# Kernel optimization log

Measured on AMD Instinct MI355X. Metric: run time of the kernel, lower is better.

Reference implementation:

```python
import jax, jax.numpy as jnp
import numpy as np

B, F, D = 16384, 64, 32
H = 256            # deep_intermediate_size
HO = 128           # higher_order_features_size
NPAIR = F * (F - 1) // 2
CIN = HO + NPAIR + D
OUT = 1


def setup_inputs() -> dict:
    key = jax.random.key(0)
    ks = jax.random.split(key, 12)
    s = 0.02
    return {
        'x':   jax.random.normal(ks[0], (B, F, D), jnp.float32),
        'W1':  jax.random.normal(ks[1], (F * D, H), jnp.float32) * s,
        'b1':  jnp.zeros((H,), jnp.float32),
        'W2':  jax.random.normal(ks[2], (H, H), jnp.float32) * s,
        'b2':  jnp.zeros((H,), jnp.float32),
        'W3':  jax.random.normal(ks[3], (H, HO), jnp.float32) * s,
        'b3':  jnp.zeros((HO,), jnp.float32),
        'Wc1': jax.random.normal(ks[4], (CIN, 256), jnp.float32) * s,
        'bc1': jnp.zeros((256,), jnp.float32),
        'Wc2': jax.random.normal(ks[5], (256, OUT), jnp.float32) * s,
        'bc2': jnp.zeros((OUT,), jnp.float32),
    }


def reference(x, W1, b1, W2, b2, W3, b3, Wc1, bc1, Wc2, bc2):
    b, f, d = x.shape
    # second-order interactions: Gram matrix + upper-triangular extraction
    # (replaces the O(F^2) python loop of bmm's in the original)
    gram = jnp.einsum('bid,bjd->bij', x, x)          # (B, F, F)
    iu, ju = jnp.triu_indices(f, k=1)                # row-major i<j order, matches the loop
    soi = gram[:, iu, ju]                            # (B, F*(F-1)/2)
    # original writes so_int into a fresh non-grad tensor -> detached
    soi = jax.lax.stop_gradient(soi)

    # deep processor (3-layer MLP with SELU; dropout inactive at eval)
    h = jax.nn.selu(x.reshape(b, f * d) @ W1 + b1)
    h = jax.nn.selu(h @ W2 + b2)
    hoi = h @ W3 + b3                                # (B, HO)

    first_order = x.sum(axis=1)                      # (B, D)

    cin = jnp.concatenate([hoi, soi, first_order], axis=1)  # (B, CIN)
    c = jax.nn.relu(cin @ Wc1 + bc1)
    return c @ Wc2 + bc2                             # (B, OUT)
```

## Files before the change

### kernel.cpp

```cpp
#include <hip/hip_runtime.h>
#include <hip/hip_bf16.h>

#define BATCH 16384
#define F_DIM 64
#define D_DIM 32
#define H_DIM 256
#define HO_DIM 128
#define NPAIR 2016
#define CIN_DIM 2176

typedef __hip_bfloat16 bf16;
using bf16x8 = __attribute__((ext_vector_type(8))) __bf16;
using f32x4  = __attribute__((ext_vector_type(4))) float;

__device__ inline float selu_f(float v) {
    const float scale = 1.0507009873554805f;
    const float alpha = 1.6732632423543772f;
    return v > 0.f ? scale * v : scale * alpha * (__expf(v) - 1.f);
}

__device__ inline void gload16(const void* g, void* l) {
    __builtin_amdgcn_global_load_lds(
        (const __attribute__((address_space(1))) void*)g,
        (__attribute__((address_space(3))) void*)l,
        16, 0, 0);
}

__global__ void prep(const float* __restrict__ W1, const float* __restrict__ W2,
                     const float* __restrict__ W3, const float* __restrict__ Wc1,
                     bf16* __restrict__ W1T, bf16* __restrict__ W2T,
                     bf16* __restrict__ W3Tsw, bf16* __restrict__ Wc1T) {
    int bid = blockIdx.x, tid = threadIdx.x;
    if (bid < 2048) {
        int i = bid * 256 + tid;
        int n = i & 255, k = i >> 8;
        W1T[(size_t)n * 2048 + k] = __float2bfloat16(W1[i]);
    } else if (bid < 2304) {
        int i = (bid - 2048) * 256 + tid;
        int n = i & 255, k = i >> 8;
        W2T[n * 256 + k] = __float2bfloat16(W2[i]);
    } else if (bid < 2432) {
        int i = (bid - 2304) * 256 + tid;
        int k = i >> 7, n = i & 127;
        W3Tsw[n * 256 + (((k >> 3) ^ (n & 7)) * 8) + (k & 7)] = __float2bfloat16(W3[i]);
    } else {
        int i = (bid - 2432) * 256 + tid;
        int n = i & 255, k = i >> 8;
        Wc1T[(size_t)n * 2176 + k] = __float2bfloat16(Wc1[i]);
    }
}

__global__ __launch_bounds__(512, 2) void gram_mlp1(
    const float* __restrict__ x, const bf16* __restrict__ W1T,
    const float* __restrict__ b1, bf16* __restrict__ cin, bf16* __restrict__ h1) {
    constexpr int K = 2048;
    __shared__ __align__(16) char smraw[81920];
    bf16* Abuf0 = (bf16*)smraw;
    bf16* Abuf1 = (bf16*)(smraw + 8192);
    bf16* Bbuf0 = (bf16*)(smraw + 16384);
    bf16* Bbuf1 = (bf16*)(smraw + 49152);

    const int tid = threadIdx.x;
    const int w = tid >> 6, l = tid & 63;
    const int lr = l & 15, lk = l >> 4;
    const int wm = w >> 2, wn = w & 3;
    const int blk = blockIdx.x;
    const int batch0 = blk * 64 + w * 8;

    bf16x8 xa[8][4];
    bf16* mysoi = (bf16*)(smraw + w * 4096);
    const int pi[10] = {0,0,0,0,1,1,1,2,2,3};
    const int pj[10] = {0,1,2,3,1,2,3,2,3,3};

    float4 pf[2][8];
#pragma unroll
    for (int ti = 0; ti < 4; ++ti) {
        const float* p = x + (size_t)batch0 * 2048 + (ti * 16 + lr) * 32 + lk * 8;
        pf[0][ti * 2]     = *(const float4*)p;
        pf[0][ti * 2 + 1] = *(const float4*)(p + 4);
    }

#pragma unroll
    for (int bb = 0; bb < 8; ++bb) {
        if (bb < 7) {
#pragma unroll
            for (int ti = 0; ti < 4; ++ti) {
                const float* p = x + (size_t)(batch0 + bb + 1) * 2048 + (ti * 16 + lr) * 32 + lk * 8;
                pf[(bb + 1) & 1][ti * 2]     = *(const float4*)p;
                pf[(bb + 1) & 1][ti * 2 + 1] = *(const float4*)(p + 4);
            }
        }
        float fsum[8];
#pragma unroll
        for (int j = 0; j < 8; ++j) fsum[j] = 0.f;
#pragma unroll
        for (int ti = 0; ti < 4; ++ti) {
            float4 f0 = pf[bb & 1][ti * 2];
            float4 f1 = pf[bb & 1][ti * 2 + 1];
            bf16x8 t;
            t[0] = (__bf16)f0.x; t[1] = (__bf16)f0.y; t[2] = (__bf16)f0.z; t[3] = (__bf16)f0.w;
            t[4] = (__bf16)f1.x; t[5] = (__bf16)f1.y; t[6] = (__bf16)f1.z; t[7] = (__bf16)f1.w;
            xa[bb][ti] = t;
            fsum[0] += f0.x; fsum[1] += f0.y; fsum[2] += f0.z; fsum[3] += f0.w;
            fsum[4] += f1.x; fsum[5] += f1.y; fsum[6] += f1.z; fsum[7] += f1.w;
        }
#pragma unroll
        for (int m = 1; m < 16; m <<= 1)
#pragma unroll
            for (int j = 0; j < 8; ++j)
                fsum[j] += __shfl_xor(fsum[j], m, 64);
        if (lr == 0) {
            bf16x8 fv;
#pragma unroll
            for (int j = 0; j < 8; ++j) fv[j] = (__bf16)fsum[j];
            *(bf16x8*)(cin + (size_t)(batch0 + bb) * CIN_DIM + (HO_DIM + NPAIR) + lk * 8) = fv;
        }
        f32x4 zero = {0.f, 0.f, 0.f, 0.f};
#pragma unroll
        for (int p = 0; p < 10; ++p) {
            f32x4 g = __builtin_amdgcn_mfma_f32_16x16x32_bf16(xa[bb][pi[p]], xa[bb][pj[p]], zero, 0, 0, 0);
            int ib = pi[p] * 16 + lk * 4;
            int j  = pj[p] * 16 + lr;
#pragma unroll
            for (int r = 0; r < 4; ++r) {
                int i = ib + r;
                if (j > i) {
                    int idx = (i * (127 - i)) / 2 + (j - i - 1);
                    mysoi[idx] = __float2bfloat16(g[r]);
                }
            }
        }
        const uint4* s4 = (const uint4*)mysoi;
        uint4* dst = (uint4*)(cin + (size_t)(batch0 + bb) * CIN_DIM + HO_DIM);
        for (int c = l; c < 252; c += 64) dst[c] = s4[c];
    }

    __syncthreads();

    const bf16* gBs[4];
#pragma unroll
    for (int s = 0; s < 4; ++s) {
        int col = s * 64 + (tid >> 3);
        gBs[s] = W1T + (size_t)col * K + (((tid & 7) ^ (col & 7)) * 8);
    }
    int aoff[2][2], boff[4][2];
#pragma unroll
    for (int fm = 0; fm < 2; ++fm) {
        int arow = wm * 32 + fm * 16 + lr;
#pragma unroll
        for (int kk = 0; kk < 2; ++kk)
            aoff[fm][kk] = arow * 64 + (((kk * 4 + lk) ^ (arow & 7)) * 8);
    }
#pragma unroll
    for (int fn = 0; fn < 4; ++fn) {
        int bcol = wn * 64 + fn * 16 + lr;
#pragma unroll
        for (int kk = 0; kk < 2; ++kk)
            boff[fn][kk] = bcol * 64 + (((kk * 4 + lk) ^ (bcol & 7)) * 8);
    }

    f32x4 acc[2][4];
#pragma unroll
    for (int fm = 0; fm < 2; ++fm)
#pragma unroll
        for (int fn = 0; fn < 4; ++fn)
            acc[fm][fn] = (f32x4){0.f, 0.f, 0.f, 0.f};

#define WRITEA(tt, DST) { \
    const int f0_ = 2 * (tt); \
    const int lrA_ = f0_ & 15, lrB_ = (f0_ + 1) & 15; \
    int delta_ = (lr == lrA_) ? 0 : ((lr == lrB_) ? 1 : -1); \
    if (delta_ >= 0) { \
        int cs_ = delta_ * 4 + lk; \
        _Pragma("unroll") \
        for (int bb_ = 0; bb_ < 8; ++bb_) { \
            int row_ = w * 8 + bb_; \
            *(bf16x8*)((DST) + row_ * 64 + ((cs_ ^ (row_ & 7)) * 8)) = xa[bb_][(tt) >> 3]; \
        } } }

    WRITEA(0, Abuf0);
#pragma unroll
    for (int s = 0; s < 4; ++s)
        gload16(gBs[s], Bbuf0 + (s * 512 + tid) * 8);
    __syncthreads();

#pragma unroll
    for (int t = 0; t < 32; ++t) {
        bf16* Ac = (t & 1) ? Abuf1 : Abuf0;
        bf16* Bc = (t & 1) ? Bbuf1 : Bbuf0;
        bf16* An = (t & 1) ? Abuf0 : Abuf1;
        bf16* Bn = (t & 1) ? Bbuf0 : Bbuf1;
        if (t < 31) {
#pragma unroll
            for (int s = 0; s < 4; ++s)
                gload16(gBs[s] + (size_t)(t + 1) * 64, Bn + (s * 512 + tid) * 8);
        }
        bf16x8 a[2][2], bfr[4][2];
#pragma unroll
        for (int fm = 0; fm < 2; ++fm)
#pragma unroll
            for (int kk = 0; kk < 2; ++kk)
                a[fm][kk] = *(const bf16x8*)(Ac + aoff[fm][kk]);
#pragma unroll
        for (int fn = 0; fn < 4; ++fn)
#pragma unroll
            for (int kk = 0; kk < 2; ++kk)
                bfr[fn][kk] = *(const bf16x8*)(Bc + boff[fn][kk]);
#pragma unroll
        for (int kk = 0; kk < 2; ++kk)
#pragma unroll
            for (int fm = 0; fm < 2; ++fm)
#pragma unroll
                for (int fn = 0; fn < 4; ++fn)
                    acc[fm][fn] = __builtin_amdgcn_mfma_f32_16x16x32_bf16(
                        a[fm][kk], bfr[fn][kk], acc[fm][fn], 0, 0, 0);
        if (t < 31) WRITEA(t + 1, An);
        __syncthreads();
    }
#undef WRITEA

#pragma unroll
    for (int fm = 0; fm < 2; ++fm) {
#pragma unroll
        for (int fn = 0; fn < 4; ++fn) {
            int col = wn * 64 + fn * 16 + lr;
            float bv = b1[col];
#pragma unroll
            for (int r = 0; r < 4; ++r) {
                float v = selu_f(acc[fm][fn][r] + bv);
                int row = blk * 64 + wm * 32 + fm * 16 + lk * 4 + r;
                h1[(size_t)row * 256 + col] = __float2bfloat16(v);
            }
        }
    }
}

__global__ __launch_bounds__(512, 2) void mlp23(
    const bf16* __restrict__ h1, const bf16* __restrict__ W2T, const float* __restrict__ b2,
    const bf16* __restrict__ W3Tsw, const float* __restrict__ b3, bf16* __restrict__ cin) {
    __shared__ __align__(16) char smraw[147456];
    bf16* Abuf0 = (bf16*)smraw;
    bf16* Abuf1 = (bf16*)(smraw + 8192);
    bf16* Bbuf0 = (bf16*)(smraw + 16384);
    bf16* Bbuf1 = (bf16*)(smraw + 49152);
    bf16* w3l   = (bf16*)(smraw + 81920);
    bf16* h2sw  = (bf16*)smraw;

    const int tid = threadIdx.x;
    const int w = tid >> 6, l = tid & 63;
    const int lr = l & 15, lk = l >> 4;
    const int wm = w >> 2, wn = w & 3;
    const int rowblk = blockIdx.x * 64;
    const int srow = tid >> 3, sks = tid & 7;

#pragma unroll
    for (int s = 0; s < 8; ++s)
        gload16(W3Tsw + (size_t)(s * 512 + tid) * 8, w3l + (s * 512 + tid) * 8);

    const bf16* gA = h1 + (size_t)(rowblk + srow) * 256 + ((sks ^ (srow & 7)) * 8);
    const bf16* gBs[4];
#pragma unroll
    for (int s = 0; s < 4; ++s) {
        int col = s * 64 + srow;
        gBs[s] = W2T + (size_t)col * 256 + ((sks ^ (col & 7)) * 8);
    }
    int aoff[2][2], boff[4][2];
#pragma unroll
    for (int fm = 0; fm < 2; ++fm) {
        int arow = wm * 32 + fm * 16 + lr;
#pragma unroll
        for (int kk = 0; kk < 2; ++kk)
            aoff[fm][kk] = arow * 64 + (((kk * 4 + lk) ^ (arow & 7)) * 8);
    }
#pragma unroll
    for (int fn = 0; fn < 4; ++fn) {
        int bcol = wn * 64 + fn * 16 + lr;
#pragma unroll
        for (int kk = 0; kk < 2; ++kk)
            boff[fn][kk] = bcol * 64 + (((kk * 4 + lk) ^ (bcol & 7)) * 8);
    }

    f32x4 acc[2][4];
#pragma unroll
    for (int fm = 0; fm < 2; ++fm)
#pragma unroll
        for (int fn = 0; fn < 4; ++fn)
            acc[fm][fn] = (f32x4){0.f, 0.f, 0.f, 0.f};

    gload16(gA, Abuf0 + tid * 8);
#pragma unroll
    for (int s = 0; s < 4; ++s)
        gload16(gBs[s], Bbuf0 + (s * 512 + tid) * 8);
    __syncthreads();

#pragma unroll
    for (int t = 0; t < 4; ++t) {
        bf16* Ac = (t & 1) ? Abuf1 : Abuf0;
        bf16* Bc = (t & 1) ? Bbuf1 : Bbuf0;
        bf16* An = (t & 1) ? Abuf0 : Abuf1;
        bf16* Bn = (t & 1) ? Bbuf0 : Bbuf1;
        if (t < 3) {
            gload16(gA + (size_t)(t + 1) * 64, An + tid * 8);
#pragma unroll
            for (int s = 0; s < 4; ++s)
                gload16(gBs[s] + (size_t)(t + 1) * 64, Bn + (s * 512 + tid) * 8);
        }
        bf16x8 a[2][2], bfr[4][2];
#pragma unroll
        for (int fm = 0; fm < 2; ++fm)
#pragma unroll
            for (int kk = 0; kk < 2; ++kk)
                a[fm][kk] = *(const bf16x8*)(Ac + aoff[fm][kk]);
#pragma unroll
        for (int fn = 0; fn < 4; ++fn)
#pragma unroll
            for (int kk = 0; kk < 2; ++kk)
                bfr[fn][kk] = *(const bf16x8*)(Bc + boff[fn][kk]);
#pragma unroll
        for (int kk = 0; kk < 2; ++kk)
#pragma unroll
            for (int fm = 0; fm < 2; ++fm)
#pragma unroll
                for (int fn = 0; fn < 4; ++fn)
                    acc[fm][fn] = __builtin_amdgcn_mfma_f32_16x16x32_bf16(
                        a[fm][kk], bfr[fn][kk], acc[fm][fn], 0, 0, 0);
        __syncthreads();
    }

#pragma unroll
    for (int fm = 0; fm < 2; ++fm) {
#pragma unroll
        for (int fn = 0; fn < 4; ++fn) {
            int col = wn * 64 + fn * 16 + lr;
            float bv = b2[col];
#pragma unroll
            for (int r = 0; r < 4; ++r) {
                float v = selu_f(acc[fm][fn][r] + bv);
                int row = wm * 32 + fm * 16 + lk * 4 + r;
                h2sw[row * 256 + (((col >> 3) ^ (row & 7)) * 8) + (col & 7)] = __float2bfloat16(v);
            }
        }
    }
    __syncthreads();

    f32x4 acc2[2][2];
#pragma unroll
    for (int fm = 0; fm < 2; ++fm)
#pragma unroll
        for (int fn = 0; fn < 2; ++fn)
            acc2[fm][fn] = (f32x4){0.f, 0.f, 0.f, 0.f};
#pragma unroll
    for (int ks = 0; ks < 8; ++ks) {
        bf16x8 a2[2], b2f[2];
#pragma unroll
        for (int fm = 0; fm < 2; ++fm) {
            int arow = wm * 32 + fm * 16 + lr;
            a2[fm] = *(const bf16x8*)(h2sw + arow * 256 + (((ks * 4 + lk) ^ (arow & 7)) * 8));
        }
#pragma unroll
        for (int fn = 0; fn < 2; ++fn) {
            int ncol = wn * 32 + fn * 16 + lr;
            b2f[fn] = *(const bf16x8*)(w3l + ncol * 256 + (((ks * 4 + lk) ^ (ncol & 7)) * 8));
        }
#pragma unroll
        for (int fm = 0; fm < 2; ++fm)
#pragma unroll
            for (int fn = 0; fn < 2; ++fn)
                acc2[fm][fn] = __builtin_amdgcn_mfma_f32_16x16x32_bf16(
                    a2[fm], b2f[fn], acc2[fm][fn], 0, 0, 0);
    }
#pragma unroll
    for (int fm = 0; fm < 2; ++fm) {
#pragma unroll
        for (int fn = 0; fn < 2; ++fn) {
            int col = wn * 32 + fn * 16 + lr;
            float bv = b3[col];
#pragma unroll
            for (int r = 0; r < 4; ++r) {
                float v = acc2[fm][fn][r] + bv;
                int row = rowblk + wm * 32 + fm * 16 + lk * 4 + r;
                cin[(size_t)row * CIN_DIM + col] = __float2bfloat16(v);
            }
        }
    }
}

template<int K, int N>
__global__ __launch_bounds__(512) void gemm_head(
    const bf16* __restrict__ A,
    const bf16* __restrict__ BT,
    const float* __restrict__ bias,
    const float* __restrict__ Wc2, const float* __restrict__ bc2,
    float* __restrict__ Out)
{
    constexpr int BK = 64;
    constexpr int NT = K / BK;
    constexpr int FN = N / 64;
    constexpr int BST = (N * 8) / 512;

    __shared__ __align__(16) bf16 Abuf[2][64 * BK];
    __shared__ __align__(16) bf16 Bbuf[2][N * BK];
    __shared__ float red[4][64];

    const int tid = threadIdx.x;
    const int w = tid >> 6, l = tid & 63;
    const int wm = w >> 2, wn = w & 3;
    const int lr = l & 15, lk = l >> 4;
    const int rowblk = blockIdx.x * 64;
    const int srow = tid >> 3, sks = tid & 7;

    const bf16* gAb = A + (size_t)(rowblk + srow) * K + ((sks ^ (srow & 7)) * 8);
    const bf16* gBs[BST];
#pragma unroll
    for (int s = 0; s < BST; ++s) {
        int col = s * 64 + srow;
        gBs[s] = BT + (size_t)col * K + ((sks ^ (col & 7)) * 8);
    }

    int aoff[2][2], boff[FN][2];
#pragma unroll
    for (int fm = 0; fm < 2; ++fm) {
        int arow = wm * 32 + fm * 16 + lr;
#pragma unroll
        for (int kk = 0; kk < 2; ++kk)
            aoff[fm][kk] = arow * BK + (((kk * 4 + lk) ^ (arow & 7)) * 8);
    }
#pragma unroll
    for (int fn = 0; fn < FN; ++fn) {
        int bcol = wn * (FN * 16) + fn * 16 + lr;
#pragma unroll
        for (int kk = 0; kk < 2; ++kk)
            boff[fn][kk] = bcol * BK + (((kk * 4 + lk) ^ (bcol & 7)) * 8);
    }

    f32x4 acc[2][FN];
#pragma unroll
    for (int fm = 0; fm < 2; ++fm)
#pragma unroll
        for (int fn = 0; fn < FN; ++fn)
            acc[fm][fn] = (f32x4){0.f, 0.f, 0.f, 0.f};

    auto stage = [&](int buf, int t) {
        gload16(gAb + (size_t)t * BK, &Abuf[buf][tid * 8]);
#pragma unroll
        for (int s = 0; s < BST; ++s)
            gload16(gBs[s] + (size_t)t * BK, &Bbuf[buf][(s * 512 + tid) * 8]);
    };

    stage(0, 0);
    __syncthreads();

    int cur = 0;
    for (int t = 0; t < NT; ++t) {
        if (t + 1 < NT) stage(cur ^ 1, t + 1);
        bf16x8 a[2][2], bfr[FN][2];
#pragma unroll
        for (int fm = 0; fm < 2; ++fm)
#pragma unroll
            for (int kk = 0; kk < 2; ++kk)
                a[fm][kk] = *(const bf16x8*)&Abuf[cur][aoff[fm][kk]];
#pragma unroll
        for (int fn = 0; fn < FN; ++fn)
#pragma unroll
            for (int kk = 0; kk < 2; ++kk)
                bfr[fn][kk] = *(const bf16x8*)&Bbuf[cur][boff[fn][kk]];
#pragma unroll
        for (int kk = 0; kk < 2; ++kk)
#pragma unroll
            for (int fm = 0; fm < 2; ++fm)
#pragma unroll
                for (int fn = 0; fn < FN; ++fn)
                    acc[fm][fn] = __builtin_amdgcn_mfma_f32_16x16x32_bf16(
                        a[fm][kk], bfr[fn][kk], acc[fm][fn], 0, 0, 0);
        __syncthreads();
        cur ^= 1;
    }

    float part[2][4];
#pragma unroll
    for (int fm = 0; fm < 2; ++fm)
#pragma unroll
        for (int r = 0; r < 4; ++r) part[fm][r] = 0.f;
#pragma unroll
    for (int fm = 0; fm < 2; ++fm) {
#pragma unroll
        for (int fn = 0; fn < FN; ++fn) {
            int col = wn * (FN * 16) + fn * 16 + lr;
            float bv = bias[col];
            float wv = Wc2[col];
#pragma unroll
            for (int r = 0; r < 4; ++r) {
                float v = acc[fm][fn][r] + bv;
                v = fmaxf(v, 0.f);
                part[fm][r] += v * wv;
            }
        }
    }
#pragma unroll
    for (int fm = 0; fm < 2; ++fm)
#pragma unroll
        for (int r = 0; r < 4; ++r)
#pragma unroll
            for (int m = 1; m < 16; m <<= 1)
                part[fm][r] += __shfl_xor(part[fm][r], m, 64);
    if (lr == 0) {
#pragma unroll
        for (int fm = 0; fm < 2; ++fm)
#pragma unroll
            for (int r = 0; r < 4; ++r)
                red[wn][wm * 32 + fm * 16 + lk * 4 + r] = part[fm][r];
    }
    __syncthreads();
    if (tid < 64)
        Out[rowblk + tid] = red[0][tid] + red[1][tid] + red[2][tid] + red[3][tid] + bc2[0];
}

extern "C" void kernel_launch(void* const* d_in, const int* in_sizes, int n_in,
                              void* d_out, int out_size, void* d_ws, size_t ws_size,
                              hipStream_t stream) {
    const float* x   = (const float*)d_in[0];
    const float* W1  = (const float*)d_in[1];
    const float* b1  = (const float*)d_in[2];
    const float* W2  = (const float*)d_in[3];
    const float* b2  = (const float*)d_in[4];
    const float* W3  = (const float*)d_in[5];
    const float* b3  = (const float*)d_in[6];
    const float* Wc1 = (const float*)d_in[7];
    const float* bc1 = (const float*)d_in[8];
    const float* Wc2 = (const float*)d_in[9];
    const float* bc2 = (const float*)d_in[10];
    float* out = (float*)d_out;

    char* ws = (char*)d_ws;
    bf16* W1T   = (bf16*)ws; ws += (size_t)256 * 2048 * 2;
    bf16* W2T   = (bf16*)ws; ws += (size_t)256 * 256 * 2;
    bf16* W3Tsw = (bf16*)ws; ws += (size_t)128 * 256 * 2;
    bf16* Wc1T  = (bf16*)ws; ws += (size_t)256 * 2176 * 2;
    bf16* h1    = (bf16*)ws; ws += (size_t)BATCH * H_DIM * 2;
    bf16* cin   = (bf16*)ws; ws += (size_t)BATCH * CIN_DIM * 2;

    prep<<<4608, 256, 0, stream>>>(W1, W2, W3, Wc1, W1T, W2T, W3Tsw, Wc1T);
    gram_mlp1<<<256, 512, 0, stream>>>(x, W1T, b1, cin, h1);
    mlp23<<<256, 512, 0, stream>>>(h1, W2T, b2, W3Tsw, b3, cin);
    gemm_head<2176, 256><<<256, 512, 0, stream>>>(cin, Wc1T, bc1, Wc2, bc2, out);
}
```

Baseline: 123.3 us.

## Fuse Gram tiles directly into head GEMM, drop materialized cin buffer

The head's first layer is split by input segment. The second-order part is computed in the gram kernel by streaming Gram tiles from LDS straight into MFMA against a padded, tile-ordered copy of Wc1, and the first-order part is added in the same pass. The partial result is stored as fp32 z. The higher-order part and the ReLU/Wc2 reduction are fused into the MLP23 kernel, which removes the large bf16 cin round trip and one launch. In exchange the padded K grows to 2560 with about 20% wasted MACs, the gram kernel uses more LDS and drops to one block per CU, and an fp32 z buffer adds traffic.

```diff
diff --git a/kernel.cpp b/kernel.cpp
--- a/kernel.cpp
+++ b/kernel.cpp
@@ -7,7 +7,7 @@
 #define H_DIM 256
 #define HO_DIM 128
 #define NPAIR 2016
-#define CIN_DIM 2176
+#define KSOI 2560
 
 typedef __hip_bfloat16 bf16;
 using bf16x8 = __attribute__((ext_vector_type(8))) __bf16;
@@ -26,10 +26,17 @@
         16, 0, 0);
 }
 
+__device__ inline int soi_swz(int dw, int row) {
+    return dw ^ (((dw >> 5) & 3) << 3) ^ ((row & 7) << 2);
+}
+
 __global__ void prep(const float* __restrict__ W1, const float* __restrict__ W2,
                      const float* __restrict__ W3, const float* __restrict__ Wc1,
                      bf16* __restrict__ W1T, bf16* __restrict__ W2T,
-                     bf16* __restrict__ W3Tsw, bf16* __restrict__ Wc1T) {
+                     bf16* __restrict__ W3Tsw, bf16* __restrict__ Wc1p,
+                     bf16* __restrict__ Wc1hT, bf16* __restrict__ Wc1fT) {
+    const int TI[10] = {0,0,0,0,1,1,1,2,2,3};
+    const int TJ[10] = {0,1,2,3,1,2,3,2,3,3};
     int bid = blockIdx.x, tid = threadIdx.x;
     if (bid < 2048) {
         int i = bid * 256 + tid;
@@ -43,22 +50,40 @@
         int i = (bid - 2304) * 256 + tid;
         int k = i >> 7, n = i & 127;
         W3Tsw[n * 256 + (((k >> 3) ^ (n & 7)) * 8) + (k & 7)] = __float2bfloat16(W3[i]);
+    } else if (bid < 2688) {
+        int n = bid - 2432;
+        for (int kp = tid; kp < KSOI; kp += 256) {
+            int t = kp >> 8, s = kp & 255;
+            int gi = TI[t] * 16 + (s >> 4);
+            int gj = TJ[t] * 16 + (s & 15);
+            float v = 0.f;
+            if (gi < gj) {
+                int pidx = (gi * (127 - gi)) / 2 + (gj - gi - 1);
+                v = Wc1[(size_t)(HO_DIM + pidx) * 256 + n];
+            }
+            Wc1p[(size_t)n * KSOI + kp] = __float2bfloat16(v);
+        }
+    } else if (bid < 2816) {
+        int i = (bid - 2688) * 256 + tid;
+        int n = i >> 7, k = i & 127;
+        Wc1hT[n * 128 + k] = __float2bfloat16(Wc1[(size_t)k * 256 + n]);
     } else {
-        int i = (bid - 2432) * 256 + tid;
-        int n = i & 255, k = i >> 8;
-        Wc1T[(size_t)n * 2176 + k] = __float2bfloat16(Wc1[i]);
+        int i = (bid - 2816) * 256 + tid;
+        int n = i >> 5, k = i & 31;
+        Wc1fT[n * 32 + k] = __float2bfloat16(Wc1[(size_t)(HO_DIM + NPAIR + k) * 256 + n]);
     }
 }
 
-__global__ __launch_bounds__(512, 2) void gram_mlp1(
-    const float* __restrict__ x, const bf16* __restrict__ W1T,
-    const float* __restrict__ b1, bf16* __restrict__ cin, bf16* __restrict__ h1) {
-    constexpr int K = 2048;
-    __shared__ __align__(16) char smraw[81920];
-    bf16* Abuf0 = (bf16*)smraw;
-    bf16* Abuf1 = (bf16*)(smraw + 8192);
-    bf16* Bbuf0 = (bf16*)(smraw + 16384);
-    bf16* Bbuf1 = (bf16*)(smraw + 49152);
+__global__ __launch_bounds__(512, 1) void gram_z_mlp1(
+    const float* __restrict__ x, const bf16* __restrict__ Wc1p,
+    const bf16* __restrict__ Wc1fT, const bf16* __restrict__ W1T,
+    const float* __restrict__ b1, float* __restrict__ z, bf16* __restrict__ h1) {
+    constexpr int TI[10] = {0,0,0,0,1,1,1,2,2,3};
+    constexpr int TJ[10] = {0,1,2,3,1,2,3,2,3,3};
+    __shared__ __align__(16) char smraw[135168];
+    bf16* Afirst = (bf16*)(smraw + 131072);
+    bf16* Bsoi0  = (bf16*)(smraw + 65536);
+    bf16* Bsoi1  = (bf16*)(smraw + 98304);
 
     const int tid = threadIdx.x;
     const int w = tid >> 6, l = tid & 63;
@@ -66,12 +91,9 @@
     const int wm = w >> 2, wn = w & 3;
     const int blk = blockIdx.x;
     const int batch0 = blk * 64 + w * 8;
+    const int srow = tid >> 3, sks = tid & 7;
 
     bf16x8 xa[8][4];
-    bf16* mysoi = (bf16*)(smraw + w * 4096);
-    const int pi[10] = {0,0,0,0,1,1,1,2,2,3};
-    const int pj[10] = {0,1,2,3,1,2,3,2,3,3};
-
     float4 pf[2][8];
 #pragma unroll
     for (int ti = 0; ti < 4; ++ti) {
@@ -79,7 +101,6 @@
         pf[0][ti * 2]     = *(const float4*)p;
         pf[0][ti * 2 + 1] = *(const float4*)(p + 4);
     }
-
 #pragma unroll
     for (int bb = 0; bb < 8; ++bb) {
         if (bb < 7) {
@@ -113,35 +134,134 @@
             bf16x8 fv;
 #pragma unroll
             for (int j = 0; j < 8; ++j) fv[j] = (__bf16)fsum[j];
-            *(bf16x8*)(cin + (size_t)(batch0 + bb) * CIN_DIM + (HO_DIM + NPAIR) + lk * 8) = fv;
-        }
+            *(bf16x8*)(Afirst + (w * 8 + bb) * 32 + lk * 8) = fv;
+        }
+    }
+
+    const bf16* gBs[4];
+#pragma unroll
+    for (int s = 0; s < 4; ++s) {
+        int col = s * 64 + srow;
+        gBs[s] = Wc1p + (size_t)col * KSOI + ((sks ^ (col & 7)) * 8);
+    }
+    {
         f32x4 zero = {0.f, 0.f, 0.f, 0.f};
 #pragma unroll
-        for (int p = 0; p < 10; ++p) {
-            f32x4 g = __builtin_amdgcn_mfma_f32_16x16x32_bf16(xa[bb][pi[p]], xa[bb][pj[p]], zero, 0, 0, 0);
-            int ib = pi[p] * 16 + lk * 4;
-            int j  = pj[p] * 16 + lr;
+        for (int bb = 0; bb < 8; ++bb) {
+            f32x4 g = __builtin_amdgcn_mfma_f32_16x16x32_bf16(xa[bb][0], xa[bb][0], zero, 0, 0, 0);
+            int rowb = w * 8 + bb;
 #pragma unroll
             for (int r = 0; r < 4; ++r) {
-                int i = ib + r;
-                if (j > i) {
-                    int idx = (i * (127 - i)) / 2 + (j - i - 1);
-                    mysoi[idx] = __float2bfloat16(g[r]);
+                int i = lk * 4 + r;
+                int dw = i * 8 + (lr >> 1);
+                *(bf16*)(smraw + rowb * 512 + soi_swz(dw, rowb) * 4 + (lr & 1) * 2) =
+                    __float2bfloat16(g[r]);
+            }
+        }
+#pragma unroll
+        for (int s = 0; s < 4; ++s)
+            gload16(gBs[s], Bsoi0 + (s * 512 + tid) * 8);
+    }
+    __syncthreads();
+
+    f32x4 acc[2][4];
+    {
+        bf16x8 af[2], bf_[4];
+#pragma unroll
+        for (int fm = 0; fm < 2; ++fm) {
+            int row = wm * 32 + fm * 16 + lr;
+            af[fm] = *(const bf16x8*)(Afirst + row * 32 + lk * 8);
+        }
+#pragma unroll
+        for (int fn = 0; fn < 4; ++fn) {
+            int col = wn * 64 + fn * 16 + lr;
+            bf_[fn] = *(const bf16x8*)(Wc1fT + col * 32 + lk * 8);
+        }
+        f32x4 zero = {0.f, 0.f, 0.f, 0.f};
+#pragma unroll
+        for (int fm = 0; fm < 2; ++fm)
+#pragma unroll
+            for (int fn = 0; fn < 4; ++fn)
+                acc[fm][fn] = __builtin_amdgcn_mfma_f32_16x16x32_bf16(af[fm], bf_[fn], zero, 0, 0, 0);
+    }
+
+#pragma unroll
+    for (int c = 0; c < 40; ++c) {
+        const int t = c >> 2;
+        char* at = smraw + ((t & 1) ? 32768 : 0);
+        bf16* Bc = (c & 1) ? Bsoi1 : Bsoi0;
+        bf16* Bn = (c & 1) ? Bsoi0 : Bsoi1;
+        if (c < 39) {
+#pragma unroll
+            for (int s = 0; s < 4; ++s)
+                gload16(gBs[s] + (c + 1) * 64, Bn + (s * 512 + tid) * 8);
+        }
+        bf16x8 a[2][2], bfr[4][2];
+#pragma unroll
+        for (int kk2 = 0; kk2 < 2; ++kk2) {
+            const int ks = (c & 3) * 2 + kk2;
+#pragma unroll
+            for (int fm = 0; fm < 2; ++fm) {
+                int row = wm * 32 + fm * 16 + lr;
+                int i = ks * 2 + (lk >> 1);
+                int dw = i * 8 + (lk & 1) * 4;
+                a[fm][kk2] = *(const bf16x8*)(at + row * 512 + soi_swz(dw, row) * 4);
+            }
+#pragma unroll
+            for (int fn = 0; fn < 4; ++fn) {
+                int bcol = wn * 64 + fn * 16 + lr;
+                bfr[fn][kk2] = *(const bf16x8*)(Bc + bcol * 64 + (((kk2 * 4 + lk) ^ (bcol & 7)) * 8));
+            }
+        }
+#pragma unroll
+        for (int kk2 = 0; kk2 < 2; ++kk2)
+#pragma unroll
+            for (int fm = 0; fm < 2; ++fm)
+#pragma unroll
+                for (int fn = 0; fn < 4; ++fn)
+                    acc[fm][fn] = __builtin_amdgcn_mfma_f32_16x16x32_bf16(
+                        a[fm][kk2], bfr[fn][kk2], acc[fm][fn], 0, 0, 0);
+        if ((c & 3) == 3 && t < 9) {
+            char* an = smraw + (((t + 1) & 1) ? 32768 : 0);
+            f32x4 zero = {0.f, 0.f, 0.f, 0.f};
+#pragma unroll
+            for (int bb = 0; bb < 8; ++bb) {
+                f32x4 g = __builtin_amdgcn_mfma_f32_16x16x32_bf16(
+                    xa[bb][TI[t + 1]], xa[bb][TJ[t + 1]], zero, 0, 0, 0);
+                int rowb = w * 8 + bb;
+#pragma unroll
+                for (int r = 0; r < 4; ++r) {
+                    int i = lk * 4 + r;
+                    int dw = i * 8 + (lr >> 1);
+                    *(bf16*)(an + rowb * 512 + soi_swz(dw, rowb) * 4 + (lr & 1) * 2) =
+                        __float2bfloat16(g[r]);
                 }
             }
         }
-        const uint4* s4 = (const uint4*)mysoi;
-        uint4* dst = (uint4*)(cin + (size_t)(batch0 + bb) * CIN_DIM + HO_DIM);
-        for (int c = l; c < 252; c += 64) dst[c] = s4[c];
-    }
-
-    __syncthreads();
-
-    const bf16* gBs[4];
+        __syncthreads();
+    }
+
+#pragma unroll
+    for (int fm = 0; fm < 2; ++fm)
+#pragma unroll
+        for (int fn = 0; fn < 4; ++fn) {
+            int col = wn * 64 + fn * 16 + lr;
+#pragma unroll
+            for (int r = 0; r < 4; ++r) {
+                int row = blk * 64 + wm * 32 + fm * 16 + lk * 4 + r;
+                z[(size_t)row * 256 + col] = acc[fm][fn][r];
+            }
+        }
+
+    bf16* Abuf0 = (bf16*)smraw;
+    bf16* Abuf1 = (bf16*)(smraw + 8192);
+    bf16* Bbuf0 = (bf16*)(smraw + 16384);
+    bf16* Bbuf1 = (bf16*)(smraw + 49152);
+    const bf16* gW1[4];
 #pragma unroll
     for (int s = 0; s < 4; ++s) {
-        int col = s * 64 + (tid >> 3);
-        gBs[s] = W1T + (size_t)col * K + (((tid & 7) ^ (col & 7)) * 8);
+        int col = s * 64 + srow;
+        gW1[s] = W1T + (size_t)col * 2048 + ((sks ^ (col & 7)) * 8);
     }
     int aoff[2][2], boff[4][2];
 #pragma unroll
@@ -159,12 +279,12 @@
             boff[fn][kk] = bcol * 64 + (((kk * 4 + lk) ^ (bcol & 7)) * 8);
     }
 
-    f32x4 acc[2][4];
+    f32x4 acm[2][4];
 #pragma unroll
     for (int fm = 0; fm < 2; ++fm)
 #pragma unroll
         for (int fn = 0; fn < 4; ++fn)
-            acc[fm][fn] = (f32x4){0.f, 0.f, 0.f, 0.f};
+            acm[fm][fn] = (f32x4){0.f, 0.f, 0.f, 0.f};
 
 #define WRITEA(tt, DST) { \
     const int f0_ = 2 * (tt); \
@@ -181,7 +301,7 @@
     WRITEA(0, Abuf0);
 #pragma unroll
     for (int s = 0; s < 4; ++s)
-        gload16(gBs[s], Bbuf0 + (s * 512 + tid) * 8);
+        gload16(gW1[s], Bbuf0 + (s * 512 + tid) * 8);
     __syncthreads();
 
 #pragma unroll
@@ -193,7 +313,7 @@
         if (t < 31) {
 #pragma unroll
             for (int s = 0; s < 4; ++s)
-                gload16(gBs[s] + (size_t)(t + 1) * 64, Bn + (s * 512 + tid) * 8);
+                gload16(gW1[s] + (size_t)(t + 1) * 64, Bn + (s * 512 + tid) * 8);
         }
         bf16x8 a[2][2], bfr[4][2];
 #pragma unroll
@@ -212,8 +332,8 @@
             for (int fm = 0; fm < 2; ++fm)
 #pragma unroll
                 for (int fn = 0; fn < 4; ++fn)
-                    acc[fm][fn] = __builtin_amdgcn_mfma_f32_16x16x32_bf16(
-                        a[fm][kk], bfr[fn][kk], acc[fm][fn], 0, 0, 0);
+                    acm[fm][fn] = __builtin_amdgcn_mfma_f32_16x16x32_bf16(
+                        a[fm][kk], bfr[fn][kk], acm[fm][fn], 0, 0, 0);
         if (t < 31) WRITEA(t + 1, An);
         __syncthreads();
     }
@@ -227,7 +347,7 @@
             float bv = b1[col];
 #pragma unroll
             for (int r = 0; r < 4; ++r) {
-                float v = selu_f(acc[fm][fn][r] + bv);
+                float v = selu_f(acm[fm][fn][r] + bv);
                 int row = blk * 64 + wm * 32 + fm * 16 + lk * 4 + r;
                 h1[(size_t)row * 256 + col] = __float2bfloat16(v);
             }
@@ -235,16 +355,21 @@
     }
 }
 
-__global__ __launch_bounds__(512, 2) void mlp23(
+__global__ __launch_bounds__(512, 1) void mlp23_head(
     const bf16* __restrict__ h1, const bf16* __restrict__ W2T, const float* __restrict__ b2,
-    const bf16* __restrict__ W3Tsw, const float* __restrict__ b3, bf16* __restrict__ cin) {
+    const bf16* __restrict__ W3Tsw, const float* __restrict__ b3,
+    const bf16* __restrict__ Wc1hT, const float* __restrict__ z,
+    const float* __restrict__ bc1, const float* __restrict__ Wc2,
+    const float* __restrict__ bc2, float* __restrict__ Out) {
     __shared__ __align__(16) char smraw[147456];
+    __shared__ float red[4][64];
     bf16* Abuf0 = (bf16*)smraw;
     bf16* Abuf1 = (bf16*)(smraw + 8192);
     bf16* Bbuf0 = (bf16*)(smraw + 16384);
     bf16* Bbuf1 = (bf16*)(smraw + 49152);
     bf16* w3l   = (bf16*)(smraw + 81920);
     bf16* h2sw  = (bf16*)smraw;
+    bf16* hoisw = (bf16*)(smraw + 49152);
 
     const int tid = threadIdx.x;
     const int w = tid >> 6, l = tid & 63;
@@ -378,120 +503,61 @@
 #pragma unroll
             for (int r = 0; r < 4; ++r) {
                 float v = acc2[fm][fn][r] + bv;
+                int row = wm * 32 + fm * 16 + lk * 4 + r;
+                hoisw[row * 128 + (((col >> 3) ^ (row & 7)) * 8) + (col & 7)] = __float2bfloat16(v);
+            }
+        }
+    }
+    __syncthreads();
+
+    f32x4 acch[2][4];
+#pragma unroll
+    for (int fm = 0; fm < 2; ++fm)
+#pragma unroll
+        for (int fn = 0; fn < 4; ++fn) {
+            int col = wn * 64 + fn * 16 + lr;
+#pragma unroll
+            for (int r = 0; r < 4; ++r) {
                 int row = rowblk + wm * 32 + fm * 16 + lk * 4 + r;
-                cin[(size_t)row * CIN_DIM + col] = __float2bfloat16(v);
-            }
-        }
-    }
-}
-
-template<int K, int N>
-__global__ __launch_bounds__(512) void gemm_head(
-    const bf16* __restrict__ A,
-    const bf16* __restrict__ BT,
-    const float* __restrict__ bias,
-    const float* __restrict__ Wc2, const float* __restrict__ bc2,
-    float* __restrict__ Out)
-{
-    constexpr int BK = 64;
-    constexpr int NT = K / BK;
-    constexpr int FN = N / 64;
-    constexpr int BST = (N * 8) / 512;
-
-    __shared__ __align__(16) bf16 Abuf[2][64 * BK];
-    __shared__ __align__(16) bf16 Bbuf[2][N * BK];
-    __shared__ float red[4][64];
-
-    const int tid = threadIdx.x;
-    const int w = tid >> 6, l = tid & 63;
-    const int wm = w >> 2, wn = w & 3;
-    const int lr = l & 15, lk = l >> 4;
-    const int rowblk = blockIdx.x * 64;
-    const int srow = tid >> 3, sks = tid & 7;
-
-    const bf16* gAb = A + (size_t)(rowblk + srow) * K + ((sks ^ (srow & 7)) * 8);
-    const bf16* gBs[BST];
-#pragma unroll
-    for (int s = 0; s < BST; ++s) {
-        int col = s * 64 + srow;
-        gBs[s] = BT + (size_t)col * K + ((sks ^ (col & 7)) * 8);
-    }
-
-    int aoff[2][2], boff[FN][2];
+                acch[fm][fn][r] = z[(size_t)row * 256 + col];
+            }
+        }
+#pragma unroll
+    for (int ks = 0; ks < 4; ++ks) {
+        bf16x8 a3[2], b3f[4];
+#pragma unroll
+        for (int fm = 0; fm < 2; ++fm) {
+            int arow = wm * 32 + fm * 16 + lr;
+            a3[fm] = *(const bf16x8*)(hoisw + arow * 128 + (((ks * 4 + lk) ^ (arow & 7)) * 8));
+        }
+#pragma unroll
+        for (int fn = 0; fn < 4; ++fn) {
+            int col = wn * 64 + fn * 16 + lr;
+            b3f[fn] = *(const bf16x8*)(Wc1hT + col * 128 + ks * 32 + lk * 8);
+        }
+#pragma unroll
+        for (int fm = 0; fm < 2; ++fm)
+#pragma unroll
+            for (int fn = 0; fn < 4; ++fn)
+                acch[fm][fn] = __builtin_amdgcn_mfma_f32_16x16x32_bf16(
+                    a3[fm], b3f[fn], acch[fm][fn], 0, 0, 0);
+    }
+
+    float part[2][4];
+#pragma unroll
+    for (int fm = 0; fm < 2; ++fm)
+#pragma unroll
+        for (int r = 0; r < 4; ++r) part[fm][r] = 0.f;
 #pragma unroll
     for (int fm = 0; fm < 2; ++fm) {
-        int arow = wm * 32 + fm * 16 + lr;
-#pragma unroll
-        for (int kk = 0; kk < 2; ++kk)
-            aoff[fm][kk] = arow * BK + (((kk * 4 + lk) ^ (arow & 7)) * 8);
-    }
-#pragma unroll
-    for (int fn = 0; fn < FN; ++fn) {
-        int bcol = wn * (FN * 16) + fn * 16 + lr;
-#pragma unroll
-        for (int kk = 0; kk < 2; ++kk)
-            boff[fn][kk] = bcol * BK + (((kk * 4 + lk) ^ (bcol & 7)) * 8);
-    }
-
-    f32x4 acc[2][FN];
-#pragma unroll
-    for (int fm = 0; fm < 2; ++fm)
-#pragma unroll
-        for (int fn = 0; fn < FN; ++fn)
-            acc[fm][fn] = (f32x4){0.f, 0.f, 0.f, 0.f};
-
-    auto stage = [&](int buf, int t) {
-        gload16(gAb + (size_t)t * BK, &Abuf[buf][tid * 8]);
-#pragma unroll
-        for (int s = 0; s < BST; ++s)
-            gload16(gBs[s] + (size_t)t * BK, &Bbuf[buf][(s * 512 + tid) * 8]);
-    };
-
-    stage(0, 0);
-    __syncthreads();
-
-    int cur = 0;
-    for (int t = 0; t < NT; ++t) {
-        if (t + 1 < NT) stage(cur ^ 1, t + 1);
-        bf16x8 a[2][2], bfr[FN][2];
-#pragma unroll
-        for (int fm = 0; fm < 2; ++fm)
-#pragma unroll
-            for (int kk = 0; kk < 2; ++kk)
-                a[fm][kk] = *(const bf16x8*)&Abuf[cur][aoff[fm][kk]];
-#pragma unroll
-        for (int fn = 0; fn < FN; ++fn)
-#pragma unroll
-            for (int kk = 0; kk < 2; ++kk)
-                bfr[fn][kk] = *(const bf16x8*)&Bbuf[cur][boff[fn][kk]];
-#pragma unroll
-        for (int kk = 0; kk < 2; ++kk)
-#pragma unroll
-            for (int fm = 0; fm < 2; ++fm)
-#pragma unroll
-                for (int fn = 0; fn < FN; ++fn)
-                    acc[fm][fn] = __builtin_amdgcn_mfma_f32_16x16x32_bf16(
-                        a[fm][kk], bfr[fn][kk], acc[fm][fn], 0, 0, 0);
-        __syncthreads();
-        cur ^= 1;
-    }
-
-    float part[2][4];
-#pragma unroll
-    for (int fm = 0; fm < 2; ++fm)
-#pragma unroll
-        for (int r = 0; r < 4; ++r) part[fm][r] = 0.f;
-#pragma unroll
-    for (int fm = 0; fm < 2; ++fm) {
-#pragma unroll
-        for (int fn = 0; fn < FN; ++fn) {
-            int col = wn * (FN * 16) + fn * 16 + lr;
-            float bv = bias[col];
+#pragma unroll
+        for (int fn = 0; fn < 4; ++fn) {
+            int col = wn * 64 + fn * 16 + lr;
+            float bv = bc1[col];
             float wv = Wc2[col];
 #pragma unroll
             for (int r = 0; r < 4; ++r) {
-                float v = acc[fm][fn][r] + bv;
-                v = fmaxf(v, 0.f);
+                float v = fmaxf(acch[fm][fn][r] + bv, 0.f);
                 part[fm][r] += v * wv;
             }
         }
@@ -535,12 +601,13 @@
     bf16* W1T   = (bf16*)ws; ws += (size_t)256 * 2048 * 2;
     bf16* W2T   = (bf16*)ws; ws += (size_t)256 * 256 * 2;
     bf16* W3Tsw = (bf16*)ws; ws += (size_t)128 * 256 * 2;
-    bf16* Wc1T  = (bf16*)ws; ws += (size_t)256 * 2176 * 2;
+    bf16* Wc1p  = (bf16*)ws; ws += (size_t)256 * KSOI * 2;
+    bf16* Wc1hT = (bf16*)ws; ws += (size_t)256 * 128 * 2;
+    bf16* Wc1fT = (bf16*)ws; ws += (size_t)256 * 32 * 2;
     bf16* h1    = (bf16*)ws; ws += (size_t)BATCH * H_DIM * 2;
-    bf16* cin   = (bf16*)ws; ws += (size_t)BATCH * CIN_DIM * 2;
-
-    prep<<<4608, 256, 0, stream>>>(W1, W2, W3, Wc1, W1T, W2T, W3Tsw, Wc1T);
-    gram_mlp1<<<256, 512, 0, stream>>>(x, W1T, b1, cin, h1);
-    mlp23<<<256, 512, 0, stream>>>(h1, W2T, b2, W3Tsw, b3, cin);
-    gemm_head<2176, 256><<<256, 512, 0, stream>>>(cin, Wc1T, bc1, Wc2, bc2, out);
+    float* z    = (float*)ws; ws += (size_t)BATCH * 256 * 4;
+
+    prep<<<2848, 256, 0, stream>>>(W1, W2, W3, Wc1, W1T, W2T, W3Tsw, Wc1p, Wc1hT, Wc1fT);
+    gram_z_mlp1<<<256, 512, 0, stream>>>(x, Wc1p, Wc1fT, W1T, b1, z, h1);
+    mlp23_head<<<256, 512, 0, stream>>>(h1, W2T, b2, W3Tsw, b3, Wc1hT, z, bc1, Wc2, bc2, out);
 }
```

After: 155.1 us. 25.8% more time.
